# Kernel optimization log

Measured on AMD Instinct MI355X. Metric: run time of the kernel, lower is better.

The kernel has to match this reference:

```python
import jax, jax.numpy as jnp
import numpy as np

N = 100000
D = 64
E = 1600000
ALPHA = 0.1
BETA = 0.5


def setup_inputs() -> dict:
    key = jax.random.key(0)
    k1, k2, k3, k4, k5, k6 = jax.random.split(key, 6)
    x = jax.random.normal(k1, (N, D), dtype=jnp.float32)
    h0 = jax.random.normal(k2, (N, D), dtype=jnp.float32)
    edge_row = jax.random.randint(k3, (E,), 0, N, dtype=jnp.int32)
    edge_col = jax.random.randint(k4, (E,), 0, N, dtype=jnp.int32)
    edge_val = jax.random.uniform(k5, (E,), dtype=jnp.float32)
    # kaiming_uniform_(a=sqrt(5)) ~= uniform(-1/sqrt(fan_in), 1/sqrt(fan_in)) up to gain; plain normal scaled is fine as a stand-in param
    bound = 1.0 / np.sqrt(D)
    weight = jax.random.uniform(k6, (D, D), dtype=jnp.float32, minval=-bound, maxval=bound)
    return {"x": x, "h0": h0, "edge_row": edge_row, "edge_col": edge_col,
            "edge_val": edge_val, "weight": weight}


def reference(x, h0, edge_row, edge_col, edge_val, weight):
    # support = (1 - alpha) * x + alpha * h0
    support = (1.0 - ALPHA) * x + ALPHA * h0  # [N, D]
    # sparse spmm: out[i] = sum_{e: row[e]==i} val[e] * support[col[e]]
    msgs = edge_val[:, None] * support[edge_col]  # [E, D]
    agg = jax.ops.segment_sum(msgs, edge_row, num_segments=N)  # [N, D]
    # convex blend with dense matmul branch
    out = (1.0 - BETA) * agg + BETA * (support @ weight)  # [N, D]
    return out
```

## Files before the change

### kernel.cpp

```cpp
#include <hip/hip_runtime.h>
#include <hip/hip_bf16.h>

#define DIM 64

__device__ __forceinline__ int   nt_i(const int* p)   { return __builtin_nontemporal_load(p); }
__device__ __forceinline__ float nt_f(const float* p) { return __builtin_nontemporal_load(p); }
__device__ __forceinline__ long long nt_ll(const void* p) {
    return __builtin_nontemporal_load((const long long*)p);
}

__global__ __launch_bounds__(256) void support_bf16_kernel(
    const float* __restrict__ x, const float* __restrict__ h0,
    __hip_bfloat16* __restrict__ sup_bf, long total4)
{
    long idx = (long)blockIdx.x * blockDim.x + threadIdx.x;
    const long stride = (long)gridDim.x * blockDim.x;
    for (long t = idx; t < total4; t += stride) {
        const float4 xv = ((const float4*)x)[t];
        const float4 hv = ((const float4*)h0)[t];
        union { ushort4 u4; __hip_bfloat16 h[4]; } cvt;
        cvt.h[0] = __float2bfloat16(0.9f * xv.x + 0.1f * hv.x);
        cvt.h[1] = __float2bfloat16(0.9f * xv.y + 0.1f * hv.y);
        cvt.h[2] = __float2bfloat16(0.9f * xv.z + 0.1f * hv.z);
        cvt.h[3] = __float2bfloat16(0.9f * xv.w + 0.1f * hv.w);
        ((ushort4*)sup_bf)[t] = cvt.u4;
    }
}

__global__ __launch_bounds__(256) void dense_gemm_kernel(
    const __hip_bfloat16* __restrict__ sup_bf,
    const float* __restrict__ weight, float* __restrict__ out, int n)
{
    __shared__ float s_tile[64][68];
    __shared__ float w_tile[64][68];

    const int tid = threadIdx.x;
    for (int i = tid; i < 64 * 64; i += 256)
        w_tile[i >> 6][i & 63] = weight[i];

    const int row0 = blockIdx.x * 64;
    for (int p = tid; p < 1024; p += 256) {
        const int r = p >> 4;
        const int c = (p & 15) << 2;
        const int row = row0 + r;
        if (row < n) {
            union { ushort4 u4; __hip_bfloat16 h[4]; } cvt;
            cvt.u4 = *(const ushort4*)&sup_bf[(size_t)row * DIM + c];
            s_tile[r][c]     = __bfloat162float(cvt.h[0]);
            s_tile[r][c + 1] = __bfloat162float(cvt.h[1]);
            s_tile[r][c + 2] = __bfloat162float(cvt.h[2]);
            s_tile[r][c + 3] = __bfloat162float(cvt.h[3]);
        } else {
            s_tile[r][c] = 0.f; s_tile[r][c+1] = 0.f;
            s_tile[r][c+2] = 0.f; s_tile[r][c+3] = 0.f;
        }
    }
    __syncthreads();

    const int tx = tid & 15, ty = tid >> 4;
    const int r0 = ty * 4, c0 = tx * 4;
    float acc[4][4] = {};
    #pragma unroll 2
    for (int k = 0; k < 64; k += 4) {
        float4 a[4], b[4];
        #pragma unroll
        for (int i = 0; i < 4; ++i) a[i] = *(const float4*)&s_tile[r0 + i][k];
        #pragma unroll
        for (int j = 0; j < 4; ++j) b[j] = *(const float4*)&w_tile[k + j][c0];
        #pragma unroll
        for (int i = 0; i < 4; ++i) {
            acc[i][0] = fmaf(a[i].x, b[0].x, acc[i][0]);
            acc[i][1] = fmaf(a[i].x, b[0].y, acc[i][1]);
            acc[i][2] = fmaf(a[i].x, b[0].z, acc[i][2]);
            acc[i][3] = fmaf(a[i].x, b[0].w, acc[i][3]);
            acc[i][0] = fmaf(a[i].y, b[1].x, acc[i][0]);
            acc[i][1] = fmaf(a[i].y, b[1].y, acc[i][1]);
            acc[i][2] = fmaf(a[i].y, b[1].z, acc[i][2]);
            acc[i][3] = fmaf(a[i].y, b[1].w, acc[i][3]);
            acc[i][0] = fmaf(a[i].z, b[2].x, acc[i][0]);
            acc[i][1] = fmaf(a[i].z, b[2].y, acc[i][1]);
            acc[i][2] = fmaf(a[i].z, b[2].z, acc[i][2]);
            acc[i][3] = fmaf(a[i].z, b[2].w, acc[i][3]);
            acc[i][0] = fmaf(a[i].w, b[3].x, acc[i][0]);
            acc[i][1] = fmaf(a[i].w, b[3].y, acc[i][1]);
            acc[i][2] = fmaf(a[i].w, b[3].z, acc[i][2]);
            acc[i][3] = fmaf(a[i].w, b[3].w, acc[i][3]);
        }
    }
    #pragma unroll
    for (int i = 0; i < 4; ++i) {
        const int row = row0 + r0 + i;
        if (row < n) {
            float4 o;
            o.x = 0.5f * acc[i][0]; o.y = 0.5f * acc[i][1];
            o.z = 0.5f * acc[i][2]; o.w = 0.5f * acc[i][3];
            *(float4*)&out[(size_t)row * DIM + c0] = o;
        }
    }
}

__global__ __launch_bounds__(256) void hist_kernel(
    const int* __restrict__ erow, int* __restrict__ counts, int e)
{
    int idx = blockIdx.x * blockDim.x + threadIdx.x;
    const int stride = gridDim.x * blockDim.x;
    for (int i = idx; i < e; i += stride)
        atomicAdd(&counts[nt_i(&erow[i])], 1);
}

__global__ __launch_bounds__(256) void scan1_kernel(
    const int* __restrict__ counts, int* __restrict__ ex,
    int* __restrict__ blockSums, int n)
{
    __shared__ int lds[256];
    const int t = threadIdx.x;
    const int base = blockIdx.x * 1024 + t * 4;
    int v[4]; int sum = 0;
    #pragma unroll
    for (int j = 0; j < 4; ++j) {
        const int idx = base + j;
        v[j] = (idx < n) ? counts[idx] : 0;
        sum += v[j];
    }
    lds[t] = sum;
    __syncthreads();
    #pragma unroll
    for (int off = 1; off < 256; off <<= 1) {
        const int y = (t >= off) ? lds[t - off] : 0;
        __syncthreads();
        lds[t] += y;
        __syncthreads();
    }
    const int excl_t = lds[t] - sum;
    if (t == 255) blockSums[blockIdx.x] = lds[255];
    int run = excl_t;
    #pragma unroll
    for (int j = 0; j < 4; ++j) {
        const int idx = base + j;
        if (idx < n) ex[idx] = run;
        run += v[j];
    }
}

__global__ __launch_bounds__(128) void scan2_kernel(int* __restrict__ bs, int nb)
{
    __shared__ int lds[128];
    const int t = threadIdx.x;
    const int v = (t < nb) ? bs[t] : 0;
    lds[t] = v;
    __syncthreads();
    #pragma unroll
    for (int off = 1; off < 128; off <<= 1) {
        const int y = (t >= off) ? lds[t - off] : 0;
        __syncthreads();
        lds[t] += y;
        __syncthreads();
    }
    if (t < nb) bs[t] = lds[t] - v;
}

__global__ __launch_bounds__(256) void scan3_kernel(
    int* __restrict__ rowStart, int* __restrict__ cursor,
    const int* __restrict__ blockSums, int n, int e)
{
    const int i = blockIdx.x * blockDim.x + threadIdx.x;
    if (i < n) {
        const int v = rowStart[i] + blockSums[i >> 10];
        rowStart[i] = v;
        cursor[i] = v;
    }
    if (i == 0) rowStart[n] = e;
}

__global__ __launch_bounds__(256) void scatter_part_kernel(
    const int* __restrict__ erow, const int* __restrict__ ecol,
    const float* __restrict__ eval_, int* __restrict__ cursor,
    int2* __restrict__ cv, int e, int rlo_chunk)
{
    const int part = blockIdx.x & 7;
    const int bip  = blockIdx.x >> 3;
    const int nbp  = gridDim.x >> 3;
    const int rlo = part * rlo_chunk;
    const int rhi = rlo + rlo_chunk;

    int idx = bip * blockDim.x + threadIdx.x;
    const int stride = nbp * blockDim.x;
    for (int i = idx; i < e; i += stride) {
        const int r = nt_i(&erow[i]);
        if (r >= rlo && r < rhi) {
            const int c = nt_i(&ecol[i]);
            const float v = nt_f(&eval_[i]);
            const int p = atomicAdd(&cursor[r], 1);
            cv[p] = make_int2(c, __float_as_int(v));
        }
    }
}

__global__ __launch_bounds__(256) void aggregate_kernel(
    const int* __restrict__ rowStart, const int2* __restrict__ cv,
    const __hip_bfloat16* __restrict__ sup_bf, float* __restrict__ out, int n)
{
    const int row = blockIdx.x * 4 + (threadIdx.x >> 6);
    if (row >= n) return;
    const int lane = threadIdx.x & 63;
    const int s = rowStart[row], e = rowStart[row + 1];
    float acc = 0.f;
    int i = s;
    for (; i + 4 <= e; i += 4) {
        const long long q0 = nt_ll(&cv[i]);
        const long long q1 = nt_ll(&cv[i + 1]);
        const long long q2 = nt_ll(&cv[i + 2]);
        const long long q3 = nt_ll(&cv[i + 3]);
        const float m0 = __bfloat162float(sup_bf[(size_t)(int)q0 * DIM + lane]);
        const float m1 = __bfloat162float(sup_bf[(size_t)(int)q1 * DIM + lane]);
        const float m2 = __bfloat162float(sup_bf[(size_t)(int)q2 * DIM + lane]);
        const float m3 = __bfloat162float(sup_bf[(size_t)(int)q3 * DIM + lane]);
        acc = fmaf(__int_as_float((int)(q0 >> 32)), m0, acc);
        acc = fmaf(__int_as_float((int)(q1 >> 32)), m1, acc);
        acc = fmaf(__int_as_float((int)(q2 >> 32)), m2, acc);
        acc = fmaf(__int_as_float((int)(q3 >> 32)), m3, acc);
    }
    for (; i < e; ++i) {
        const long long q0 = nt_ll(&cv[i]);
        acc = fmaf(__int_as_float((int)(q0 >> 32)),
                   __bfloat162float(sup_bf[(size_t)(int)q0 * DIM + lane]), acc);
    }
    const size_t base = (size_t)row * DIM + lane;
    out[base] = fmaf(0.5f, acc, out[base]);
}

__global__ __launch_bounds__(256) void support_f32_kernel(
    const float* __restrict__ x, const float* __restrict__ h0,
    float* __restrict__ sup, long total4)
{
    long idx = (long)blockIdx.x * blockDim.x + threadIdx.x;
    const long stride = (long)gridDim.x * blockDim.x;
    for (long t = idx; t < total4; t += stride) {
        const float4 xv = ((const float4*)x)[t];
        const float4 hv = ((const float4*)h0)[t];
        float4 s;
        s.x = 0.9f * xv.x + 0.1f * hv.x;
        s.y = 0.9f * xv.y + 0.1f * hv.y;
        s.z = 0.9f * xv.z + 0.1f * hv.z;
        s.w = 0.9f * xv.w + 0.1f * hv.w;
        ((float4*)sup)[t] = s;
    }
}

__global__ __launch_bounds__(256) void dense_gemm_f32_kernel(
    const float* __restrict__ sup, const float* __restrict__ weight,
    float* __restrict__ out, int n)
{
    __shared__ float s_tile[64][68];
    __shared__ float w_tile[64][68];
    const int tid = threadIdx.x;
    for (int i = tid; i < 64 * 64; i += 256)
        w_tile[i >> 6][i & 63] = weight[i];
    const int row0 = blockIdx.x * 64;
    for (int p = tid; p < 2048; p += 256) {
        const int r = p >> 5;
        const int c = (p & 31) << 1;
        const int row = row0 + r;
        float2 s2 = make_float2(0.f, 0.f);
        if (row < n) s2 = *(const float2*)&sup[(size_t)row * DIM + c];
        s_tile[r][c] = s2.x; s_tile[r][c + 1] = s2.y;
    }
    __syncthreads();
    const int tx = tid & 15, ty = tid >> 4;
    const int r0 = ty * 4, c0 = tx * 4;
    float acc[4][4] = {};
    #pragma unroll 2
    for (int k = 0; k < 64; k += 4) {
        float4 a[4], b[4];
        #pragma unroll
        for (int i = 0; i < 4; ++i) a[i] = *(const float4*)&s_tile[r0 + i][k];
        #pragma unroll
        for (int j = 0; j < 4; ++j) b[j] = *(const float4*)&w_tile[k + j][c0];
        #pragma unroll
        for (int i = 0; i < 4; ++i) {
            acc[i][0] = fmaf(a[i].x, b[0].x, acc[i][0]);
            acc[i][1] = fmaf(a[i].x, b[0].y, acc[i][1]);
            acc[i][2] = fmaf(a[i].x, b[0].z, acc[i][2]);
            acc[i][3] = fmaf(a[i].x, b[0].w, acc[i][3]);
            acc[i][0] = fmaf(a[i].y, b[1].x, acc[i][0]);
            acc[i][1] = fmaf(a[i].y, b[1].y, acc[i][1]);
            acc[i][2] = fmaf(a[i].y, b[1].z, acc[i][2]);
            acc[i][3] = fmaf(a[i].y, b[1].w, acc[i][3]);
            acc[i][0] = fmaf(a[i].z, b[2].x, acc[i][0]);
            acc[i][1] = fmaf(a[i].z, b[2].y, acc[i][1]);
            acc[i][2] = fmaf(a[i].z, b[2].z, acc[i][2]);
            acc[i][3] = fmaf(a[i].z, b[2].w, acc[i][3]);
            acc[i][0] = fmaf(a[i].w, b[3].x, acc[i][0]);
            acc[i][1] = fmaf(a[i].w, b[3].y, acc[i][1]);
            acc[i][2] = fmaf(a[i].w, b[3].z, acc[i][2]);
            acc[i][3] = fmaf(a[i].w, b[3].w, acc[i][3]);
        }
    }
    #pragma unroll
    for (int i = 0; i < 4; ++i) {
        const int row = row0 + r0 + i;
        if (row < n) {
            float4 o;
            o.x = 0.5f * acc[i][0]; o.y = 0.5f * acc[i][1];
            o.z = 0.5f * acc[i][2]; o.w = 0.5f * acc[i][3];
            *(float4*)&out[(size_t)row * DIM + c0] = o;
        }
    }
}

__global__ __launch_bounds__(256) void spmm_atomic_kernel(
    const int* __restrict__ erow, const int* __restrict__ ecol,
    const float* __restrict__ eval_, const float* __restrict__ support,
    float* __restrict__ out, int e)
{
    const long total = (long)e * DIM;
    long idx = (long)blockIdx.x * blockDim.x + threadIdx.x;
    const long stride = (long)gridDim.x * blockDim.x;
    for (long t = idx; t < total; t += stride) {
        const int edge = (int)(t >> 6);
        const int j = (int)(t & 63);
        const float m = 0.5f * eval_[edge] * support[(long)ecol[edge] * DIM + j];
        atomicAdd(&out[(long)erow[edge] * DIM + j], m);
    }
}

extern "C" void kernel_launch(void* const* d_in, const int* in_sizes, int n_in,
                              void* d_out, int out_size, void* d_ws, size_t ws_size,
                              hipStream_t stream) {
    const float* x      = (const float*)d_in[0];
    const float* h0     = (const float*)d_in[1];
    const int*   erow   = (const int*)d_in[2];
    const int*   ecol   = (const int*)d_in[3];
    const float* eval_  = (const float*)d_in[4];
    const float* weight = (const float*)d_in[5];
    float* out = (float*)d_out;

    const int n = in_sizes[0] / DIM;
    const int e = in_sizes[2];

    char* wsb = (char*)d_ws;
    size_t off = 0;
    auto alloc = [&](size_t bytes) { size_t o = off; off = (off + bytes + 255) & ~255ULL; return o; };
    const size_t o_supbf = alloc((size_t)n * DIM * 2);
    const size_t o_cv    = alloc((size_t)e * 8);
    const size_t o_rowst = alloc((size_t)(n + 1) * 4);
    const size_t o_curs  = alloc((size_t)n * 4);
    const size_t o_cnts  = alloc((size_t)n * 4);
    const size_t o_bsums = alloc(512);
    const size_t need = off;

    const int nb1 = (n + 1023) / 1024;
    const long total4 = (long)n * DIM / 4;

    if (ws_size >= need && nb1 <= 128) {
        __hip_bfloat16* sup_bf = (__hip_bfloat16*)(wsb + o_supbf);
        int2* cv      = (int2*)(wsb + o_cv);
        int* rowStart = (int*)(wsb + o_rowst);
        int* cursor   = (int*)(wsb + o_curs);
        int* counts   = (int*)(wsb + o_cnts);
        int* bsums    = (int*)(wsb + o_bsums);

        hipMemsetAsync(counts, 0, (size_t)n * 4, stream);

        support_bf16_kernel<<<2048, 256, 0, stream>>>(x, h0, sup_bf, total4);
        hist_kernel<<<2048, 256, 0, stream>>>(erow, counts, e);
        scan1_kernel<<<nb1, 256, 0, stream>>>(counts, rowStart, bsums, n);
        scan2_kernel<<<1, 128, 0, stream>>>(bsums, nb1);
        scan3_kernel<<<(n + 255) / 256, 256, 0, stream>>>(rowStart, cursor, bsums, n, e);

        dense_gemm_kernel<<<(n + 63) / 64, 256, 0, stream>>>(sup_bf, weight, out, n);

        const int rchunk = (n + 7) / 8;
        scatter_part_kernel<<<4096, 256, 0, stream>>>(erow, ecol, eval_, cursor, cv, e, rchunk);

        aggregate_kernel<<<(n + 3) / 4, 256, 0, stream>>>(rowStart, cv, sup_bf, out, n);
    } else {
        float* support = (float*)d_ws;
        support_f32_kernel<<<2048, 256, 0, stream>>>(x, h0, support, total4);
        dense_gemm_f32_kernel<<<(n + 63) / 64, 256, 0, stream>>>(support, weight, out, n);
        spmm_atomic_kernel<<<16384, 256, 0, stream>>>(erow, ecol, eval_, support, out, e);
    }
}
```

Measured before the change: 358.9 us.

## Restructure aggregate to process four edges per wavefront with vectorized bf16 gathers

The aggregate kernel now splits each 64-lane wavefront into four groups of 16 lanes. Each group handles a different edge and gathers 4 bf16 values (8 bytes) per lane, and the four partial sums are combined with cross-lane shuffles before a float4 read-modify-write of the output. This replaces one 2-byte gather per lane per edge and is meant to raise memory-level parallelism and cut instruction count. The 0.5 blend factor is folded into edge values during scatter, bf16 conversion uses a cheap bit shift, and the histogram kernel is unrolled by four. The cost is extra shuffle reductions and wasted lanes in the tail for rows with few edges.

```diff
diff --git a/kernel.cpp b/kernel.cpp
--- a/kernel.cpp
+++ b/kernel.cpp
@@ -5,8 +5,8 @@
 
 __device__ __forceinline__ int   nt_i(const int* p)   { return __builtin_nontemporal_load(p); }
 __device__ __forceinline__ float nt_f(const float* p) { return __builtin_nontemporal_load(p); }
-__device__ __forceinline__ long long nt_ll(const void* p) {
-    return __builtin_nontemporal_load((const long long*)p);
+__device__ __forceinline__ float bfbits(unsigned short u) {
+    return __uint_as_float(((unsigned)u) << 16);
 }
 
 __global__ __launch_bounds__(256) void support_bf16_kernel(
@@ -44,12 +44,11 @@
         const int c = (p & 15) << 2;
         const int row = row0 + r;
         if (row < n) {
-            union { ushort4 u4; __hip_bfloat16 h[4]; } cvt;
-            cvt.u4 = *(const ushort4*)&sup_bf[(size_t)row * DIM + c];
-            s_tile[r][c]     = __bfloat162float(cvt.h[0]);
-            s_tile[r][c + 1] = __bfloat162float(cvt.h[1]);
-            s_tile[r][c + 2] = __bfloat162float(cvt.h[2]);
-            s_tile[r][c + 3] = __bfloat162float(cvt.h[3]);
+            const ushort4 u = *(const ushort4*)&sup_bf[(size_t)row * DIM + c];
+            s_tile[r][c]     = bfbits(u.x);
+            s_tile[r][c + 1] = bfbits(u.y);
+            s_tile[r][c + 2] = bfbits(u.z);
+            s_tile[r][c + 3] = bfbits(u.w);
         } else {
             s_tile[r][c] = 0.f; s_tile[r][c+1] = 0.f;
             s_tile[r][c+2] = 0.f; s_tile[r][c+3] = 0.f;
@@ -102,9 +101,20 @@
 __global__ __launch_bounds__(256) void hist_kernel(
     const int* __restrict__ erow, int* __restrict__ counts, int e)
 {
+    const int e4 = e >> 2;
     int idx = blockIdx.x * blockDim.x + threadIdx.x;
     const int stride = gridDim.x * blockDim.x;
-    for (int i = idx; i < e; i += stride)
+    for (int i = idx; i < e4; i += stride) {
+        const int r0 = nt_i(&erow[i * 4]);
+        const int r1 = nt_i(&erow[i * 4 + 1]);
+        const int r2 = nt_i(&erow[i * 4 + 2]);
+        const int r3 = nt_i(&erow[i * 4 + 3]);
+        atomicAdd(&counts[r0], 1);
+        atomicAdd(&counts[r1], 1);
+        atomicAdd(&counts[r2], 1);
+        atomicAdd(&counts[r3], 1);
+    }
+    for (int i = (e4 << 2) + idx; i < e; i += stride)
         atomicAdd(&counts[nt_i(&erow[i])], 1);
 }
 
@@ -189,7 +199,7 @@
         const int r = nt_i(&erow[i]);
         if (r >= rlo && r < rhi) {
             const int c = nt_i(&ecol[i]);
-            const float v = nt_f(&eval_[i]);
+            const float v = 0.5f * nt_f(&eval_[i]);
             const int p = atomicAdd(&cursor[r], 1);
             cv[p] = make_int2(c, __float_as_int(v));
         }
@@ -203,30 +213,58 @@
     const int row = blockIdx.x * 4 + (threadIdx.x >> 6);
     if (row >= n) return;
     const int lane = threadIdx.x & 63;
+    const int g   = lane >> 4;
+    const int sub = lane & 15;
+
     const int s = rowStart[row], e = rowStart[row + 1];
-    float acc = 0.f;
+    float4 acc = make_float4(0.f, 0.f, 0.f, 0.f);
+
     int i = s;
-    for (; i + 4 <= e; i += 4) {
-        const long long q0 = nt_ll(&cv[i]);
-        const long long q1 = nt_ll(&cv[i + 1]);
-        const long long q2 = nt_ll(&cv[i + 2]);
-        const long long q3 = nt_ll(&cv[i + 3]);
-        const float m0 = __bfloat162float(sup_bf[(size_t)(int)q0 * DIM + lane]);
-        const float m1 = __bfloat162float(sup_bf[(size_t)(int)q1 * DIM + lane]);
-        const float m2 = __bfloat162float(sup_bf[(size_t)(int)q2 * DIM + lane]);
-        const float m3 = __bfloat162float(sup_bf[(size_t)(int)q3 * DIM + lane]);
-        acc = fmaf(__int_as_float((int)(q0 >> 32)), m0, acc);
-        acc = fmaf(__int_as_float((int)(q1 >> 32)), m1, acc);
-        acc = fmaf(__int_as_float((int)(q2 >> 32)), m2, acc);
-        acc = fmaf(__int_as_float((int)(q3 >> 32)), m3, acc);
-    }
-    for (; i < e; ++i) {
-        const long long q0 = nt_ll(&cv[i]);
-        acc = fmaf(__int_as_float((int)(q0 >> 32)),
-                   __bfloat162float(sup_bf[(size_t)(int)q0 * DIM + lane]), acc);
-    }
-    const size_t base = (size_t)row * DIM + lane;
-    out[base] = fmaf(0.5f, acc, out[base]);
+    #define AGG_BUNDLE_FULL(ii)                                               \
+    {                                                                         \
+        const int2 q = cv[(ii) + g];                                          \
+        const float v = __int_as_float(q.y);                                  \
+        const ushort4 u = *(const ushort4*)&sup_bf[(size_t)q.x * DIM + sub * 4]; \
+        acc.x = fmaf(v, bfbits(u.x), acc.x);                                  \
+        acc.y = fmaf(v, bfbits(u.y), acc.y);                                  \
+        acc.z = fmaf(v, bfbits(u.z), acc.z);                                  \
+        acc.w = fmaf(v, bfbits(u.w), acc.w);                                  \
+    }
+    for (; i + 8 <= e; i += 8) {
+        AGG_BUNDLE_FULL(i);
+        AGG_BUNDLE_FULL(i + 4);
+    }
+    if (i + 4 <= e) {
+        AGG_BUNDLE_FULL(i);
+        i += 4;
+    }
+    if (i < e) {
+        const int idx = i + g;
+        const int2 q = cv[min(idx, e - 1)];
+        const float v = (idx < e) ? __int_as_float(q.y) : 0.f;
+        const ushort4 u = *(const ushort4*)&sup_bf[(size_t)q.x * DIM + sub * 4];
+        acc.x = fmaf(v, bfbits(u.x), acc.x);
+        acc.y = fmaf(v, bfbits(u.y), acc.y);
+        acc.z = fmaf(v, bfbits(u.z), acc.z);
+        acc.w = fmaf(v, bfbits(u.w), acc.w);
+    }
+    #undef AGG_BUNDLE_FULL
+
+    acc.x += __shfl_xor(acc.x, 16, 64);
+    acc.y += __shfl_xor(acc.y, 16, 64);
+    acc.z += __shfl_xor(acc.z, 16, 64);
+    acc.w += __shfl_xor(acc.w, 16, 64);
+    acc.x += __shfl_xor(acc.x, 32, 64);
+    acc.y += __shfl_xor(acc.y, 32, 64);
+    acc.z += __shfl_xor(acc.z, 32, 64);
+    acc.w += __shfl_xor(acc.w, 32, 64);
+
+    if (g == 0) {
+        float4* po = (float4*)&out[(size_t)row * DIM + sub * 4];
+        float4 o = *po;
+        o.x += acc.x; o.y += acc.y; o.z += acc.z; o.w += acc.w;
+        *po = o;
+    }
 }
 
 __global__ __launch_bounds__(256) void support_f32_kernel(
@@ -360,7 +398,7 @@
         int* counts   = (int*)(wsb + o_cnts);
         int* bsums    = (int*)(wsb + o_bsums);
 
-        hipMemsetAsync(counts, 0, (size_t)n * 4, stream);
+        (void)hipMemsetAsync(counts, 0, (size_t)n * 4, stream);
 
         support_bf16_kernel<<<2048, 256, 0, stream>>>(x, h0, sup_bf, total4);
         hist_kernel<<<2048, 256, 0, stream>>>(erow, counts, e);
```

After: 323.4 us. 1.11x faster.

## Bucket edges by 32-row blocks with LDS histogram and shared-memory aggregation

Applied to the files above, without the earlier changes.

Replaces the per-row CSR build with coarse 32-row buckets. The histogram now accumulates in LDS before flushing to global memory, and the scatter drops the 8-way partitioned multi-pass over all edges in favour of one pass with atomics on a few thousand bucket cursors. Each edge packs its local row into the upper bits of the column index. Aggregation runs one block per bucket, accumulating rows with LDS float atomics. This removes the per-row scan and repeated edge reads, but adds LDS atomic contention and hot global cursors, and limits n to 2^17.

```diff
diff --git a/kernel.cpp b/kernel.cpp
--- a/kernel.cpp
+++ b/kernel.cpp
@@ -2,11 +2,13 @@
 #include <hip/hip_bf16.h>
 
 #define DIM 64
+#define RPB 32
+#define MAXNB 4096
 
 __device__ __forceinline__ int   nt_i(const int* p)   { return __builtin_nontemporal_load(p); }
 __device__ __forceinline__ float nt_f(const float* p) { return __builtin_nontemporal_load(p); }
-__device__ __forceinline__ long long nt_ll(const void* p) {
-    return __builtin_nontemporal_load((const long long*)p);
+__device__ __forceinline__ float bfbits(unsigned short u) {
+    return __uint_as_float(((unsigned)u) << 16);
 }
 
 __global__ __launch_bounds__(256) void support_bf16_kernel(
@@ -44,12 +46,11 @@
         const int c = (p & 15) << 2;
         const int row = row0 + r;
         if (row < n) {
-            union { ushort4 u4; __hip_bfloat16 h[4]; } cvt;
-            cvt.u4 = *(const ushort4*)&sup_bf[(size_t)row * DIM + c];
-            s_tile[r][c]     = __bfloat162float(cvt.h[0]);
-            s_tile[r][c + 1] = __bfloat162float(cvt.h[1]);
-            s_tile[r][c + 2] = __bfloat162float(cvt.h[2]);
-            s_tile[r][c + 3] = __bfloat162float(cvt.h[3]);
+            const ushort4 u = *(const ushort4*)&sup_bf[(size_t)row * DIM + c];
+            s_tile[r][c]     = bfbits(u.x);
+            s_tile[r][c + 1] = bfbits(u.y);
+            s_tile[r][c + 2] = bfbits(u.z);
+            s_tile[r][c + 3] = bfbits(u.w);
         } else {
             s_tile[r][c] = 0.f; s_tile[r][c+1] = 0.f;
             s_tile[r][c+2] = 0.f; s_tile[r][c+3] = 0.f;
@@ -99,13 +100,21 @@
     }
 }
 
-__global__ __launch_bounds__(256) void hist_kernel(
-    const int* __restrict__ erow, int* __restrict__ counts, int e)
-{
-    int idx = blockIdx.x * blockDim.x + threadIdx.x;
-    const int stride = gridDim.x * blockDim.x;
+__global__ __launch_bounds__(256) void hist_bucket_kernel(
+    const int* __restrict__ erow, int* __restrict__ counts, int e, int nb)
+{
+    __shared__ int h[MAXNB];
+    for (int i = threadIdx.x; i < nb; i += 256) h[i] = 0;
+    __syncthreads();
+    int idx = blockIdx.x * 256 + threadIdx.x;
+    const int stride = gridDim.x * 256;
     for (int i = idx; i < e; i += stride)
-        atomicAdd(&counts[nt_i(&erow[i])], 1);
+        atomicAdd(&h[nt_i(&erow[i]) >> 5], 1);
+    __syncthreads();
+    for (int i = threadIdx.x; i < nb; i += 256) {
+        const int v = h[i];
+        if (v) atomicAdd(&counts[i], v);
+    }
 }
 
 __global__ __launch_bounds__(256) void scan1_kernel(
@@ -160,73 +169,88 @@
 }
 
 __global__ __launch_bounds__(256) void scan3_kernel(
-    int* __restrict__ rowStart, int* __restrict__ cursor,
+    int* __restrict__ bStart, int* __restrict__ cursor,
     const int* __restrict__ blockSums, int n, int e)
 {
     const int i = blockIdx.x * blockDim.x + threadIdx.x;
     if (i < n) {
-        const int v = rowStart[i] + blockSums[i >> 10];
-        rowStart[i] = v;
+        const int v = bStart[i] + blockSums[i >> 10];
+        bStart[i] = v;
         cursor[i] = v;
     }
-    if (i == 0) rowStart[n] = e;
-}
-
-__global__ __launch_bounds__(256) void scatter_part_kernel(
+    if (i == 0) bStart[n] = e;
+}
+
+__global__ __launch_bounds__(256) void scatter_bucket_kernel(
     const int* __restrict__ erow, const int* __restrict__ ecol,
     const float* __restrict__ eval_, int* __restrict__ cursor,
-    int2* __restrict__ cv, int e, int rlo_chunk)
-{
-    const int part = blockIdx.x & 7;
-    const int bip  = blockIdx.x >> 3;
-    const int nbp  = gridDim.x >> 3;
-    const int rlo = part * rlo_chunk;
-    const int rhi = rlo + rlo_chunk;
-
-    int idx = bip * blockDim.x + threadIdx.x;
-    const int stride = nbp * blockDim.x;
+    int2* __restrict__ cv, int e)
+{
+    int idx = blockIdx.x * 256 + threadIdx.x;
+    const int stride = gridDim.x * 256;
     for (int i = idx; i < e; i += stride) {
         const int r = nt_i(&erow[i]);
-        if (r >= rlo && r < rhi) {
-            const int c = nt_i(&ecol[i]);
-            const float v = nt_f(&eval_[i]);
-            const int p = atomicAdd(&cursor[r], 1);
-            cv[p] = make_int2(c, __float_as_int(v));
-        }
-    }
-}
-
-__global__ __launch_bounds__(256) void aggregate_kernel(
-    const int* __restrict__ rowStart, const int2* __restrict__ cv,
+        const int c = nt_i(&ecol[i]);
+        const float v = 0.5f * nt_f(&eval_[i]);
+        const int p = atomicAdd(&cursor[r >> 5], 1);
+        cv[p] = make_int2(((r & (RPB - 1)) << 17) | c, __float_as_int(v));
+    }
+}
+
+__global__ __launch_bounds__(256) void aggregate_bucket_kernel(
+    const int* __restrict__ bStart, const int2* __restrict__ cv,
     const __hip_bfloat16* __restrict__ sup_bf, float* __restrict__ out, int n)
 {
-    const int row = blockIdx.x * 4 + (threadIdx.x >> 6);
-    if (row >= n) return;
-    const int lane = threadIdx.x & 63;
-    const int s = rowStart[row], e = rowStart[row + 1];
-    float acc = 0.f;
-    int i = s;
-    for (; i + 4 <= e; i += 4) {
-        const long long q0 = nt_ll(&cv[i]);
-        const long long q1 = nt_ll(&cv[i + 1]);
-        const long long q2 = nt_ll(&cv[i + 2]);
-        const long long q3 = nt_ll(&cv[i + 3]);
-        const float m0 = __bfloat162float(sup_bf[(size_t)(int)q0 * DIM + lane]);
-        const float m1 = __bfloat162float(sup_bf[(size_t)(int)q1 * DIM + lane]);
-        const float m2 = __bfloat162float(sup_bf[(size_t)(int)q2 * DIM + lane]);
-        const float m3 = __bfloat162float(sup_bf[(size_t)(int)q3 * DIM + lane]);
-        acc = fmaf(__int_as_float((int)(q0 >> 32)), m0, acc);
-        acc = fmaf(__int_as_float((int)(q1 >> 32)), m1, acc);
-        acc = fmaf(__int_as_float((int)(q2 >> 32)), m2, acc);
-        acc = fmaf(__int_as_float((int)(q3 >> 32)), m3, acc);
-    }
-    for (; i < e; ++i) {
-        const long long q0 = nt_ll(&cv[i]);
-        acc = fmaf(__int_as_float((int)(q0 >> 32)),
-                   __bfloat162float(sup_bf[(size_t)(int)q0 * DIM + lane]), acc);
-    }
-    const size_t base = (size_t)row * DIM + lane;
-    out[base] = fmaf(0.5f, acc, out[base]);
+    __shared__ float acc[RPB][68];
+    const int tid = threadIdx.x;
+    for (int i = tid; i < RPB * 64; i += 256) acc[i >> 6][i & 63] = 0.f;
+    __syncthreads();
+
+    const int b = blockIdx.x;
+    const int s = bStart[b], e = bStart[b + 1];
+    const int wid = tid >> 6, lane = tid & 63;
+    const int g = lane >> 4, sub = lane & 15;
+
+    int i = s + wid * 4;
+    for (; i + 4 <= e; i += 16) {
+        const int2 q = cv[i + g];
+        const int c  = q.x & 0x1FFFF;
+        const int rl = (q.x >> 17) & (RPB - 1);
+        const float v = __int_as_float(q.y);
+        const ushort4 u = *(const ushort4*)&sup_bf[(size_t)c * DIM + sub * 4];
+        atomicAdd(&acc[rl][sub * 4 + 0], v * bfbits(u.x));
+        atomicAdd(&acc[rl][sub * 4 + 1], v * bfbits(u.y));
+        atomicAdd(&acc[rl][sub * 4 + 2], v * bfbits(u.z));
+        atomicAdd(&acc[rl][sub * 4 + 3], v * bfbits(u.w));
+    }
+    if (i < e) {
+        const int idx2 = i + g;
+        if (idx2 < e) {
+            const int2 q = cv[idx2];
+            const int c  = q.x & 0x1FFFF;
+            const int rl = (q.x >> 17) & (RPB - 1);
+            const float v = __int_as_float(q.y);
+            const ushort4 u = *(const ushort4*)&sup_bf[(size_t)c * DIM + sub * 4];
+            atomicAdd(&acc[rl][sub * 4 + 0], v * bfbits(u.x));
+            atomicAdd(&acc[rl][sub * 4 + 1], v * bfbits(u.y));
+            atomicAdd(&acc[rl][sub * 4 + 2], v * bfbits(u.z));
+            atomicAdd(&acc[rl][sub * 4 + 3], v * bfbits(u.w));
+        }
+    }
+    __syncthreads();
+
+    const int row0 = b * RPB;
+    for (int p = tid; p < RPB * 16; p += 256) {
+        const int r = p >> 4, c4 = (p & 15) << 2;
+        const int row = row0 + r;
+        if (row < n) {
+            float4* po = (float4*)&out[(size_t)row * DIM + c4];
+            float4 o = *po;
+            o.x += acc[r][c4];     o.y += acc[r][c4 + 1];
+            o.z += acc[r][c4 + 2]; o.w += acc[r][c4 + 3];
+            *po = o;
+        }
+    }
 }
 
 __global__ __launch_bounds__(256) void support_f32_kernel(
@@ -337,43 +361,43 @@
 
     const int n = in_sizes[0] / DIM;
     const int e = in_sizes[2];
+    const int nb = (n + RPB - 1) / RPB;
 
     char* wsb = (char*)d_ws;
     size_t off = 0;
     auto alloc = [&](size_t bytes) { size_t o = off; off = (off + bytes + 255) & ~255ULL; return o; };
     const size_t o_supbf = alloc((size_t)n * DIM * 2);
     const size_t o_cv    = alloc((size_t)e * 8);
-    const size_t o_rowst = alloc((size_t)(n + 1) * 4);
-    const size_t o_curs  = alloc((size_t)n * 4);
-    const size_t o_cnts  = alloc((size_t)n * 4);
+    const size_t o_bst   = alloc((size_t)(nb + 1) * 4);
+    const size_t o_curs  = alloc((size_t)nb * 4);
+    const size_t o_cnts  = alloc((size_t)nb * 4);
     const size_t o_bsums = alloc(512);
     const size_t need = off;
 
-    const int nb1 = (n + 1023) / 1024;
+    const int nb1 = (nb + 1023) / 1024;
     const long total4 = (long)n * DIM / 4;
 
-    if (ws_size >= need && nb1 <= 128) {
+    if (ws_size >= need && nb <= MAXNB && n <= (1 << 17)) {
         __hip_bfloat16* sup_bf = (__hip_bfloat16*)(wsb + o_supbf);
-        int2* cv      = (int2*)(wsb + o_cv);
-        int* rowStart = (int*)(wsb + o_rowst);
-        int* cursor   = (int*)(wsb + o_curs);
-        int* counts   = (int*)(wsb + o_cnts);
-        int* bsums    = (int*)(wsb + o_bsums);
-
-        hipMemsetAsync(counts, 0, (size_t)n * 4, stream);
+        int2* cv    = (int2*)(wsb + o_cv);
+        int* bStart = (int*)(wsb + o_bst);
+        int* cursor = (int*)(wsb + o_curs);
+        int* counts = (int*)(wsb + o_cnts);
+        int* bsums  = (int*)(wsb + o_bsums);
+
+        (void)hipMemsetAsync(counts, 0, (size_t)nb * 4, stream);
 
         support_bf16_kernel<<<2048, 256, 0, stream>>>(x, h0, sup_bf, total4);
-        hist_kernel<<<2048, 256, 0, stream>>>(erow, counts, e);
-        scan1_kernel<<<nb1, 256, 0, stream>>>(counts, rowStart, bsums, n);
+        hist_bucket_kernel<<<512, 256, 0, stream>>>(erow, counts, e, nb);
+        scan1_kernel<<<nb1, 256, 0, stream>>>(counts, bStart, bsums, nb);
         scan2_kernel<<<1, 128, 0, stream>>>(bsums, nb1);
-        scan3_kernel<<<(n + 255) / 256, 256, 0, stream>>>(rowStart, cursor, bsums, n, e);
+        scan3_kernel<<<(nb + 255) / 256, 256, 0, stream>>>(bStart, cursor, bsums, nb, e);
 
         dense_gemm_kernel<<<(n + 63) / 64, 256, 0, stream>>>(sup_bf, weight, out, n);
 
-        const int rchunk = (n + 7) / 8;
-        scatter_part_kernel<<<4096, 256, 0, stream>>>(erow, ecol, eval_, cursor, cv, e, rchunk);
-
-        aggregate_kernel<<<(n + 3) / 4, 256, 0, stream>>>(rowStart, cv, sup_bf, out, n);
+        scatter_bucket_kernel<<<2048, 256, 0, stream>>>(erow, ecol, eval_, cursor, cv, e);
+
+        aggregate_bucket_kernel<<<nb, 256, 0, stream>>>(bStart, cv, sup_bf, out, n);
     } else {
         float* support = (float*)d_ws;
         support_f32_kernel<<<2048, 256, 0, stream>>>(x, h0, support, total4);
```

Measured after the change: 848.7 us. 2.36x slower.
